# Optimization experiments

Measured on AMD Instinct MI355X. Metric: run time of the kernel, lower is better.

## Reference

```python
import jax, jax.numpy as jnp
import numpy as np
from jax import lax

BN_EPS = 1e-5

def _conv1d_same(x, w):
    # x: [N, 1, C], w: [1, 1, k] with k odd -> SAME padding along channel axis
    k = w.shape[-1]
    return lax.conv_general_dilated(x, w, window_strides=(1,),
                                    padding=[(k // 2, k // 2)],
                                    dimension_numbers=('NCH', 'OIH', 'NCH'))

def setup_inputs() -> dict:
    key = jax.random.key(0)
    ks = jax.random.split(key, 6)
    B, C, H, W = 4, 64, 64, 64
    kk = 3  # kernel size from in_dim=64: t=int(abs(log2(64)+1)/2)=3 (odd)
    x = jax.random.normal(ks[0], (B, C, H, W), dtype=jnp.float32)
    q_w = jax.random.normal(ks[1], (1, 1, kk), dtype=jnp.float32) * 0.5
    k_w = jax.random.normal(ks[2], (1, 1, kk), dtype=jnp.float32) * 0.5
    v_w = jax.random.normal(ks[3], (C, C), dtype=jnp.float32) * (1.0 / np.sqrt(C))
    v_b = jnp.zeros((C,), dtype=jnp.float32)
    gamma = jax.random.uniform(ks[4], (1,), dtype=jnp.float32, minval=0.5, maxval=1.5)
    bn_w = jnp.ones((C,), dtype=jnp.float32)
    bn_b = jnp.zeros((C,), dtype=jnp.float32)
    return {"x": x, "q_w": q_w, "k_w": k_w, "v_w": v_w, "v_b": v_b,
            "gamma": gamma, "bn_w": bn_w, "bn_b": bn_b}

def reference(x, q_w, k_w, v_w, v_b, gamma, bn_w, bn_b):
    B, C, H, W = x.shape
    N = H * W
    # conv1d Q/K projections over the channel axis, per spatial position
    xp = x.reshape(B, C, N).transpose(0, 2, 1).reshape(B * N, 1, C)
    q = _conv1d_same(xp, q_w).reshape(B, N, C)   # proj_query: [B, HW, C]
    k = _conv1d_same(xp, k_w).reshape(B, N, C)   # proj_key (pre-permute)
    energy = jnp.einsum('bnc,bmc->bnm', q, k)    # [B, HW, HW]
    attn = jax.nn.softmax(energy, axis=-1)
    # 1x1 value conv
    v = jnp.einsum('oc,bchw->bohw', v_w, x) + v_b[None, :, None, None]
    vv = v.reshape(B, C, N)
    # bmm(value, attention^T)
    out = jnp.einsum('bcm,bnm->bcn', vv, attn).reshape(B, C, H, W)
    y = gamma[0] * out
    # BatchNorm2d, training mode (batch statistics, biased variance)
    mean = jnp.mean(y, axis=(0, 2, 3), keepdims=True)
    var = jnp.var(y, axis=(0, 2, 3), keepdims=True)
    y = (y - mean) * lax.rsqrt(var + BN_EPS)
    y = y * bn_w[None, :, None, None] + bn_b[None, :, None, None]
    return y + x
```

## Files before the change

kernel.cpp:

```cpp
#include <hip/hip_runtime.h>
#include <stdint.h>

using f16 = _Float16;

typedef _Float16 f16x8 __attribute__((ext_vector_type(8)));
typedef float f32x4 __attribute__((ext_vector_type(4)));

#define LOG2E 1.44269504088896340736f

__device__ __forceinline__ f16 f2h(float f) { return (f16)f; }

#if __has_builtin(__builtin_amdgcn_exp2f)
__device__ __forceinline__ float fexp2(float x) { return __builtin_amdgcn_exp2f(x); }
#else
__device__ __forceinline__ float fexp2(float x) { return exp2f(x); }
#endif

typedef __attribute__((address_space(1))) const uint32_t gu32;
typedef __attribute__((address_space(3))) uint32_t lu32;

__device__ __forceinline__ void dma16(const void* g, void* l) {
  __builtin_amdgcn_global_load_lds((gu32*)g, (lu32*)l, 16, 0, 0);
}

__device__ __forceinline__ f16x8 cvt8(const float* p) {
  const float4 a = *(const float4*)p;
  const float4 b = *(const float4*)(p + 4);
  f16x8 r;
  r[0] = (f16)a.x; r[1] = (f16)a.y; r[2] = (f16)a.z; r[3] = (f16)a.w;
  r[4] = (f16)b.x; r[5] = (f16)b.y; r[6] = (f16)b.z; r[7] = (f16)b.w;
  return r;
}


__global__ __launch_bounds__(256, 2) void pam_pre(
    const float* __restrict__ x, const float* __restrict__ qw,
    const float* __restrict__ kw, const float* __restrict__ vw,
    const float* __restrict__ vb,
    f16* __restrict__ qa, f16* __restrict__ ka2, f16* __restrict__ va2,
    float* __restrict__ gz)
{
  __shared__ alignas(16) f16 xt[32 * 72];
  const int tid = threadIdx.x;
  const int b = blockIdx.x >> 7;
  const int n0 = (blockIdx.x & 127) << 5;
  const int lane = tid & 63;
  const int wv = tid >> 6;
  const int quad = lane >> 4, l15 = lane & 15;

  if (blockIdx.x == 0 && tid < 128) gz[tid] = 0.f;

  {
    const int c = tid >> 2;
    const int j0 = (tid & 3) << 3;
    const float* xp = x + ((size_t)(b * 64 + c) << 12) + n0 + j0;
    const float4 v0 = *(const float4*)xp;
    const float4 v1 = *(const float4*)(xp + 4);
    xt[(j0 + 0) * 72 + c] = f2h(v0.x);
    xt[(j0 + 1) * 72 + c] = f2h(v0.y);
    xt[(j0 + 2) * 72 + c] = f2h(v0.z);
    xt[(j0 + 3) * 72 + c] = f2h(v0.w);
    xt[(j0 + 4) * 72 + c] = f2h(v1.x);
    xt[(j0 + 5) * 72 + c] = f2h(v1.y);
    xt[(j0 + 6) * 72 + c] = f2h(v1.z);
    xt[(j0 + 7) * 72 + c] = f2h(v1.w);
  }
  __syncthreads();

  const float qw0 = qw[0], qw1 = qw[1], qw2 = qw[2];
  const float kw0 = kw[0], kw1 = kw[1], kw2 = kw[2];
  for (int p = 0; p < 8; ++p) {
    const int c = lane;
    const int jr = (p << 2) + wv;
    const int n = n0 + jr;
    const float xm = (c > 0) ? (float)xt[jr * 72 + c - 1] : 0.f;
    const float x0 = (float)xt[jr * 72 + c];
    const float xp = (c < 63) ? (float)xt[jr * 72 + c + 1] : 0.f;
    const float qv = (qw0 * xm + qw1 * x0 + qw2 * xp) * LOG2E;
    const float kv = kw0 * xm + kw1 * x0 + kw2 * xp;
    qa[((size_t)((b << 12) + n) << 6) + c] = f2h(qv);
    ka2[((size_t)(b * 8 + (c >> 3)) << 15) + (n << 3) + (c & 7)] = f2h(kv);
  }

  {
    const f16x8 a0 = cvt8(vw + (wv * 16 + l15) * 64 + quad * 8);
    const f16x8 a1 = cvt8(vw + (wv * 16 + l15) * 64 + quad * 8 + 32);
    f32x4 acc[2];
    for (int st = 0; st < 2; ++st) {
      const f16x8 b0 = *(const f16x8*)&xt[(st * 16 + l15) * 72 + quad * 8];
      const f16x8 b1 = *(const f16x8*)&xt[(st * 16 + l15) * 72 + quad * 8 + 32];
      f32x4 z = {0.f, 0.f, 0.f, 0.f};
      z = __builtin_amdgcn_mfma_f32_16x16x32_f16(a0, b0, z, 0, 0, 0);
      acc[st] = __builtin_amdgcn_mfma_f32_16x16x32_f16(a1, b1, z, 0, 0, 0);
    }
    const int cobase = wv * 16 + quad * 4;
    for (int st = 0; st < 2; ++st)
      for (int r = 0; r < 4; ++r) {
        const int co = cobase + r;
        const int n = n0 + st * 16 + l15;
        const float val = acc[st][r] + vb[co];
        va2[((size_t)(b * 512 + (n >> 3)) << 9) + (co << 3) + (n & 7)] = f2h(val);
      }
  }
}

__global__ __launch_bounds__(1024) void pam_attn(
    const f16* __restrict__ qa, const f16* __restrict__ ka2,
    const f16* __restrict__ va2, const float* __restrict__ gam,
    float* __restrict__ y0, float* __restrict__ gs1, float* __restrict__ gs2)
{
  __shared__ alignas(16) f16 kbuf[2][8192];
  __shared__ alignas(16) f16 vbuf[2][8192];
  __shared__ alignas(16) f16 pbuf[16][512];
  __shared__ float ldsO[64 * 65];
  __shared__ float ldsM[4][64], ldsL[4][64], ldsMg[64], ldsInv[64];

  const int tid = threadIdx.x;
  const int wv = tid >> 6, lane = tid & 63;
  const int quad = lane >> 4, l15 = lane & 15;
  const int qt = wv & 3, ks = wv >> 2;
  const int b = blockIdx.x & 3;
  const int qb = blockIdx.x >> 2;
  const int qb0 = qb << 6;
  const int phase = qb & 31;

  for (int i = tid; i < 64 * 65; i += 1024) ldsO[i] = 0.f;

  const int bn = b << 12;
  f16x8 bq0, bq1;
  {
    const int q = qb0 + qt * 16 + l15;
    const f16* qp = qa + ((size_t)(bn + q) << 6) + quad * 8;
    bq0 = *(const f16x8*)qp;
    bq1 = *(const f16x8*)(qp + 32);
  }

  const int k_c8 = tid >> 7, k_key = tid & 127;
  const f16* kg0 = ka2 + (((size_t)(b * 8 + k_c8)) << 15) + (k_key << 3);
  const int v_kc = tid >> 6, v_c = tid & 63;
  const f16* vg0 = va2 + (((size_t)(b * 512 + v_kc)) << 9) + (v_c << 3);

  const int ak_base = (((quad << 7) + ks * 32 + l15) << 3);
  const int bv_base = (((((ks << 2) + quad) << 6) + l15) << 3);

  f32x4 o[4] = {};
  float m = -1e30f, lp = 0.f;
  f16* pb = pbuf[wv];
  const int sw = l15 & 3;

  dma16(kg0 + ((size_t)phase << 10), kbuf[0] + (wv << 9));
  dma16(vg0 + ((size_t)phase << 13), vbuf[0] + (wv << 9));
  __syncthreads();

#pragma unroll 1
  for (int kt = 0; kt < 32; ++kt) {
    const int cur = kt & 1;
    {
      const int tn = (kt + 1 + phase) & 31;
      dma16(kg0 + ((size_t)tn << 10), kbuf[cur ^ 1] + (wv << 9));
      dma16(vg0 + ((size_t)tn << 13), vbuf[cur ^ 1] + (wv << 9));
    }

    const f16* kc_ = kbuf[cur];
    const f16* vc_ = vbuf[cur];
    const f16x8 ak00 = *(const f16x8*)(kc_ + ak_base);
    const f16x8 ak01 = *(const f16x8*)(kc_ + ak_base + 4096);
    const f16x8 ak10 = *(const f16x8*)(kc_ + ak_base + 128);
    const f16x8 ak11 = *(const f16x8*)(kc_ + ak_base + 128 + 4096);
    f16x8 bv[4];
    for (int ct = 0; ct < 4; ++ct)
      bv[ct] = *(const f16x8*)(vc_ + bv_base + ct * 128);

    f32x4 s0, s1;
    {
      f32x4 z = {0.f, 0.f, 0.f, 0.f};
      z = __builtin_amdgcn_mfma_f32_16x16x32_f16(ak00, bq0, z, 0, 0, 0);
      s0 = __builtin_amdgcn_mfma_f32_16x16x32_f16(ak01, bq1, z, 0, 0, 0);
    }
    {
      f32x4 z = {0.f, 0.f, 0.f, 0.f};
      z = __builtin_amdgcn_mfma_f32_16x16x32_f16(ak10, bq0, z, 0, 0, 0);
      s1 = __builtin_amdgcn_mfma_f32_16x16x32_f16(ak11, bq1, z, 0, 0, 0);
    }

    float tmax = fmaxf(fmaxf(fmaxf(s0[0], s0[1]), fmaxf(s0[2], s0[3])),
                       fmaxf(fmaxf(s1[0], s1[1]), fmaxf(s1[2], s1[3])));
    tmax = fmaxf(tmax, __shfl_xor(tmax, 16, 64));
    tmax = fmaxf(tmax, __shfl_xor(tmax, 32, 64));
    const bool upd = tmax > m;
    const float mnew = upd ? tmax : m;

    char* rowp = (char*)pb + l15 * 64;
    float tsum = 0.f;
    {
      const float p0 = fexp2(s0[0] - mnew);
      const float p1 = fexp2(s0[1] - mnew);
      const float p2 = fexp2(s0[2] - mnew);
      const float p3 = fexp2(s0[3] - mnew);
      tsum += (p0 + p1) + (p2 + p3);
      union { f16 h[4]; uint2 u; } pk;
      pk.h[0] = f2h(p0); pk.h[1] = f2h(p1);
      pk.h[2] = f2h(p2); pk.h[3] = f2h(p3);
      const int cc = (quad >> 1) ^ sw;
      *(uint2*)(rowp + cc * 16 + (quad & 1) * 8) = pk.u;
    }
    {
      const float p0 = fexp2(s1[0] - mnew);
      const float p1 = fexp2(s1[1] - mnew);
      const float p2 = fexp2(s1[2] - mnew);
      const float p3 = fexp2(s1[3] - mnew);
      tsum += (p0 + p1) + (p2 + p3);
      union { f16 h[4]; uint2 u; } pk;
      pk.h[0] = f2h(p0); pk.h[1] = f2h(p1);
      pk.h[2] = f2h(p2); pk.h[3] = f2h(p3);
      const int cc = (2 + (quad >> 1)) ^ sw;
      *(uint2*)(rowp + cc * 16 + (quad & 1) * 8) = pk.u;
    }

    if (__any(upd)) {
      const float alpha = fexp2(m - mnew);
      lp = lp * alpha + tsum;
      const int srcbase = (lane & 48) + ((lane >> 4) << 2);
      for (int r = 0; r < 4; ++r) {
        const float ar = __shfl(alpha, srcbase + r, 64);
        for (int ct = 0; ct < 4; ++ct) o[ct][r] *= ar;
      }
    } else {
      lp += tsum;
    }
    m = mnew;
    __builtin_amdgcn_s_waitcnt(0xC07F);

    const f16x8 ap =
        *(const f16x8*)((const char*)pb + l15 * 64 + ((quad ^ sw) << 4));
    for (int ct = 0; ct < 4; ++ct)
      o[ct] = __builtin_amdgcn_mfma_f32_16x16x32_f16(ap, bv[ct], o[ct], 0, 0, 0);

    __syncthreads();
  }

  {
    float v = lp;
    v += __shfl_xor(v, 16, 64);
    v += __shfl_xor(v, 32, 64);
    if (quad == 0) {
      ldsM[ks][qt * 16 + l15] = m;
      ldsL[ks][qt * 16 + l15] = v;
    }
  }
  __syncthreads();

  if (tid < 64) {
    const float M = fmaxf(fmaxf(ldsM[0][tid], ldsM[1][tid]),
                          fmaxf(ldsM[2][tid], ldsM[3][tid]));
    const float lt = ldsL[0][tid] * fexp2(ldsM[0][tid] - M) +
                     ldsL[1][tid] * fexp2(ldsM[1][tid] - M) +
                     ldsL[2][tid] * fexp2(ldsM[2][tid] - M) +
                     ldsL[3][tid] * fexp2(ldsM[3][tid] - M);
    ldsMg[tid] = M;
    ldsInv[tid] = 1.f / lt;
  }
  __syncthreads();

  for (int r = 0; r < 4; ++r) {
    const int q = qt * 16 + quad * 4 + r;
    const float sc = fexp2(ldsM[ks][q] - ldsMg[q]);
    for (int ct = 0; ct < 4; ++ct)
      atomicAdd(&ldsO[q * 65 + ct * 16 + l15], o[ct][r] * sc);
  }
  __syncthreads();

  const float g = gam[0];
  {
    const int c = tid >> 4;
    const int q0 = (tid & 15) << 2;
    float4 v4;
    float* vp = &v4.x;
    float s1 = 0.f, s2 = 0.f;
    for (int r = 0; r < 4; ++r) {
      const float val = g * ldsO[(q0 + r) * 65 + c] * ldsInv[q0 + r];
      vp[r] = val; s1 += val; s2 += val * val;
    }
    *(float4*)(y0 + ((size_t)(b * 64 + c) << 12) + qb0 + q0) = v4;
    s1 += __shfl_xor(s1, 1, 64);
    s2 += __shfl_xor(s2, 1, 64);
    s1 += __shfl_xor(s1, 2, 64);
    s2 += __shfl_xor(s2, 2, 64);
    s1 += __shfl_xor(s1, 4, 64);
    s2 += __shfl_xor(s2, 4, 64);
    s1 += __shfl_xor(s1, 8, 64);
    s2 += __shfl_xor(s2, 8, 64);
    if (l15 == 0) {
      atomicAdd(&gs1[c], s1);
      atomicAdd(&gs2[c], s2);
    }
  }
}

__global__ __launch_bounds__(256, 2) void pam_apply(
    const float* __restrict__ y0, const float* __restrict__ x,
    const float* __restrict__ gs1, const float* __restrict__ gs2,
    const float* __restrict__ bnw, const float* __restrict__ bnb,
    float* __restrict__ out)
{
  const int i = (blockIdx.x * 256 + threadIdx.x) << 2;
  const int c = (i >> 12) & 63;
  const float inv_n = 1.f / 16384.f;
  const float mean = gs1[c] * inv_n;
  const float var = fmaxf(gs2[c] * inv_n - mean * mean, 0.f);
  const float sc = bnw[c] * rsqrtf(var + 1e-5f);
  const float sh = bnb[c] - mean * sc;
  const float4 y = *(const float4*)(y0 + i);
  const float4 xv = *(const float4*)(x + i);
  float4 r;
  r.x = y.x * sc + sh + xv.x;
  r.y = y.y * sc + sh + xv.y;
  r.z = y.z * sc + sh + xv.z;
  r.w = y.w * sc + sh + xv.w;
  *(float4*)(out + i) = r;
}

extern "C" void kernel_launch(void* const* d_in, const int* in_sizes, int n_in,
                              void* d_out, int out_size, void* d_ws, size_t ws_size,
                              hipStream_t stream)
{
  (void)in_sizes; (void)n_in; (void)out_size; (void)ws_size;
  const float* x   = (const float*)d_in[0];
  const float* qw  = (const float*)d_in[1];
  const float* kw  = (const float*)d_in[2];
  const float* vw  = (const float*)d_in[3];
  const float* vb  = (const float*)d_in[4];
  const float* gam = (const float*)d_in[5];
  const float* bnw = (const float*)d_in[6];
  const float* bnb = (const float*)d_in[7];

  char* ws = (char*)d_ws;
  f16*   qa  = (f16*)(ws);
  f16*   ka2 = (f16*)(ws + (2u << 20));
  f16*   va2 = (f16*)(ws + (4u << 20));
  float* y0  = (float*)(ws + (6u << 20));
  float* gs1 = (float*)(ws + (10u << 20));
  float* gs2 = (float*)(ws + (10u << 20) + 256);

  pam_pre  <<<512, 256, 0, stream>>>(x, qw, kw, vw, vb, qa, ka2, va2, gs1);
  pam_attn <<<256, 1024, 0, stream>>>(qa, ka2, va2, gam, y0, gs1, gs2);
  pam_apply<<<1024, 256, 0, stream>>>(y0, x, gs1, gs2, bnw, bnb, (float*)d_out);
}
```

Before: 162.5 us.

## Keep softmax probabilities in registers and double key tile per iteration

The attention kernel now processes 256-key tiles over 16 iterations. Each wave handles two query tiles against 32 keys, so each K/V fragment loaded from LDS is reused twice. Probabilities are fed directly from the MFMA accumulator layout into 16x16x16 MFMAs as the A operand, which removes the per-wave P round-trip through LDS. The V layout is changed to groups of 4 keys to match that operand shape. Risks include doubled LDS staging buffers (about 128KB), more registers for two accumulator sets, and an 8-way cross-wave merge instead of 4.

```diff
diff --git a/kernel.cpp b/kernel.cpp
--- a/kernel.cpp
+++ b/kernel.cpp
@@ -4,6 +4,7 @@
 using f16 = _Float16;
 
 typedef _Float16 f16x8 __attribute__((ext_vector_type(8)));
+typedef _Float16 f16x4 __attribute__((ext_vector_type(4)));
 typedef float f32x4 __attribute__((ext_vector_type(4)));
 
 #define LOG2E 1.44269504088896340736f
@@ -37,7 +38,7 @@
     const float* __restrict__ x, const float* __restrict__ qw,
     const float* __restrict__ kw, const float* __restrict__ vw,
     const float* __restrict__ vb,
-    f16* __restrict__ qa, f16* __restrict__ ka2, f16* __restrict__ va2,
+    f16* __restrict__ qa, f16* __restrict__ ka2, f16* __restrict__ va3,
     float* __restrict__ gz)
 {
   __shared__ alignas(16) f16 xt[32 * 72];
@@ -99,174 +100,175 @@
         const int co = cobase + r;
         const int n = n0 + st * 16 + l15;
         const float val = acc[st][r] + vb[co];
-        va2[((size_t)(b * 512 + (n >> 3)) << 9) + (co << 3) + (n & 7)] = f2h(val);
-      }
-  }
-}
-
-__global__ __launch_bounds__(1024) void pam_attn(
+        va3[(((size_t)(b * 1024 + (n >> 2))) << 8) + (co << 2) + (n & 3)] = f2h(val);
+      }
+  }
+}
+
+__global__ __launch_bounds__(1024, 4) void pam_attn(
     const f16* __restrict__ qa, const f16* __restrict__ ka2,
-    const f16* __restrict__ va2, const float* __restrict__ gam,
+    const f16* __restrict__ va3, const float* __restrict__ gam,
     float* __restrict__ y0, float* __restrict__ gs1, float* __restrict__ gs2)
 {
-  __shared__ alignas(16) f16 kbuf[2][8192];
-  __shared__ alignas(16) f16 vbuf[2][8192];
-  __shared__ alignas(16) f16 pbuf[16][512];
+  __shared__ alignas(16) f16 kbuf[2][16384];
+  __shared__ alignas(16) f16 vbuf[2][16384];
   __shared__ float ldsO[64 * 65];
-  __shared__ float ldsM[4][64], ldsL[4][64], ldsMg[64], ldsInv[64];
+  __shared__ float ldsM[8][64], ldsL[8][64], ldsMg[64], ldsInv[64];
 
   const int tid = threadIdx.x;
   const int wv = tid >> 6, lane = tid & 63;
   const int quad = lane >> 4, l15 = lane & 15;
-  const int qt = wv & 3, ks = wv >> 2;
+  const int ks = wv & 7, qh = wv >> 3;
   const int b = blockIdx.x & 3;
   const int qb = blockIdx.x >> 2;
   const int qb0 = qb << 6;
-  const int phase = qb & 31;
+  const int phase = qb & 15;
 
   for (int i = tid; i < 64 * 65; i += 1024) ldsO[i] = 0.f;
 
   const int bn = b << 12;
-  f16x8 bq0, bq1;
-  {
-    const int q = qb0 + qt * 16 + l15;
+  f16x8 bq[2][2];
+  for (int qt = 0; qt < 2; ++qt) {
+    const int q = qb0 + (qh * 2 + qt) * 16 + l15;
     const f16* qp = qa + ((size_t)(bn + q) << 6) + quad * 8;
-    bq0 = *(const f16x8*)qp;
-    bq1 = *(const f16x8*)(qp + 32);
-  }
-
-  const int k_c8 = tid >> 7, k_key = tid & 127;
-  const f16* kg0 = ka2 + (((size_t)(b * 8 + k_c8)) << 15) + (k_key << 3);
-  const int v_kc = tid >> 6, v_c = tid & 63;
-  const f16* vg0 = va2 + (((size_t)(b * 512 + v_kc)) << 9) + (v_c << 3);
-
-  const int ak_base = (((quad << 7) + ks * 32 + l15) << 3);
-  const int bv_base = (((((ks << 2) + quad) << 6) + l15) << 3);
-
-  f32x4 o[4] = {};
-  float m = -1e30f, lp = 0.f;
-  f16* pb = pbuf[wv];
-  const int sw = l15 & 3;
-
-  dma16(kg0 + ((size_t)phase << 10), kbuf[0] + (wv << 9));
-  dma16(vg0 + ((size_t)phase << 13), vbuf[0] + (wv << 9));
+    bq[qt][0] = *(const f16x8*)qp;
+    bq[qt][1] = *(const f16x8*)(qp + 32);
+  }
+
+  const int k_c8 = wv >> 1;
+  const int k_koff = (wv & 1) << 7;
+  const f16* kg0 = ka2 + (((size_t)(b * 8 + k_c8)) << 15) + (k_koff << 3) + (lane << 3);
+  const int kl_base = k_c8 * 2048 + (k_koff << 3);
+  const f16* vg0 = va3 + ((size_t)b << 18) + ((wv * 64 + lane) << 3);
+  const int vl_base = wv << 9;
+
+  f32x4 o[2][4] = {};
+  float m[2] = {-1e30f, -1e30f};
+  float lp[2] = {0.f, 0.f};
+
+  dma16(kg0 + ((size_t)phase << 11),        kbuf[0] + kl_base);
+  dma16(kg0 + ((size_t)phase << 11) + 512,  kbuf[0] + kl_base + 512);
+  dma16(vg0 + ((size_t)phase << 14),        vbuf[0] + vl_base);
+  dma16(vg0 + ((size_t)phase << 14) + 8192, vbuf[0] + vl_base + 8192);
   __syncthreads();
 
 #pragma unroll 1
-  for (int kt = 0; kt < 32; ++kt) {
+  for (int kt = 0; kt < 16; ++kt) {
     const int cur = kt & 1;
     {
-      const int tn = (kt + 1 + phase) & 31;
-      dma16(kg0 + ((size_t)tn << 10), kbuf[cur ^ 1] + (wv << 9));
-      dma16(vg0 + ((size_t)tn << 13), vbuf[cur ^ 1] + (wv << 9));
-    }
-
-    const f16* kc_ = kbuf[cur];
-    const f16* vc_ = vbuf[cur];
-    const f16x8 ak00 = *(const f16x8*)(kc_ + ak_base);
-    const f16x8 ak01 = *(const f16x8*)(kc_ + ak_base + 4096);
-    const f16x8 ak10 = *(const f16x8*)(kc_ + ak_base + 128);
-    const f16x8 ak11 = *(const f16x8*)(kc_ + ak_base + 128 + 4096);
-    f16x8 bv[4];
-    for (int ct = 0; ct < 4; ++ct)
-      bv[ct] = *(const f16x8*)(vc_ + bv_base + ct * 128);
-
-    f32x4 s0, s1;
-    {
-      f32x4 z = {0.f, 0.f, 0.f, 0.f};
-      z = __builtin_amdgcn_mfma_f32_16x16x32_f16(ak00, bq0, z, 0, 0, 0);
-      s0 = __builtin_amdgcn_mfma_f32_16x16x32_f16(ak01, bq1, z, 0, 0, 0);
-    }
-    {
-      f32x4 z = {0.f, 0.f, 0.f, 0.f};
-      z = __builtin_amdgcn_mfma_f32_16x16x32_f16(ak10, bq0, z, 0, 0, 0);
-      s1 = __builtin_amdgcn_mfma_f32_16x16x32_f16(ak11, bq1, z, 0, 0, 0);
-    }
-
-    float tmax = fmaxf(fmaxf(fmaxf(s0[0], s0[1]), fmaxf(s0[2], s0[3])),
-                       fmaxf(fmaxf(s1[0], s1[1]), fmaxf(s1[2], s1[3])));
-    tmax = fmaxf(tmax, __shfl_xor(tmax, 16, 64));
-    tmax = fmaxf(tmax, __shfl_xor(tmax, 32, 64));
-    const bool upd = tmax > m;
-    const float mnew = upd ? tmax : m;
-
-    char* rowp = (char*)pb + l15 * 64;
-    float tsum = 0.f;
-    {
-      const float p0 = fexp2(s0[0] - mnew);
-      const float p1 = fexp2(s0[1] - mnew);
-      const float p2 = fexp2(s0[2] - mnew);
-      const float p3 = fexp2(s0[3] - mnew);
-      tsum += (p0 + p1) + (p2 + p3);
-      union { f16 h[4]; uint2 u; } pk;
-      pk.h[0] = f2h(p0); pk.h[1] = f2h(p1);
-      pk.h[2] = f2h(p2); pk.h[3] = f2h(p3);
-      const int cc = (quad >> 1) ^ sw;
-      *(uint2*)(rowp + cc * 16 + (quad & 1) * 8) = pk.u;
-    }
-    {
-      const float p0 = fexp2(s1[0] - mnew);
-      const float p1 = fexp2(s1[1] - mnew);
-      const float p2 = fexp2(s1[2] - mnew);
-      const float p3 = fexp2(s1[3] - mnew);
-      tsum += (p0 + p1) + (p2 + p3);
-      union { f16 h[4]; uint2 u; } pk;
-      pk.h[0] = f2h(p0); pk.h[1] = f2h(p1);
-      pk.h[2] = f2h(p2); pk.h[3] = f2h(p3);
-      const int cc = (2 + (quad >> 1)) ^ sw;
-      *(uint2*)(rowp + cc * 16 + (quad & 1) * 8) = pk.u;
-    }
-
-    if (__any(upd)) {
-      const float alpha = fexp2(m - mnew);
-      lp = lp * alpha + tsum;
-      const int srcbase = (lane & 48) + ((lane >> 4) << 2);
-      for (int r = 0; r < 4; ++r) {
-        const float ar = __shfl(alpha, srcbase + r, 64);
-        for (int ct = 0; ct < 4; ++ct) o[ct][r] *= ar;
-      }
-    } else {
-      lp += tsum;
-    }
-    m = mnew;
-    __builtin_amdgcn_s_waitcnt(0xC07F);
-
-    const f16x8 ap =
-        *(const f16x8*)((const char*)pb + l15 * 64 + ((quad ^ sw) << 4));
-    for (int ct = 0; ct < 4; ++ct)
-      o[ct] = __builtin_amdgcn_mfma_f32_16x16x32_f16(ap, bv[ct], o[ct], 0, 0, 0);
-
+      const int tn = (kt + 1 + phase) & 15;
+      f16* kd = kbuf[cur ^ 1] + kl_base;
+      f16* vd = vbuf[cur ^ 1] + vl_base;
+      dma16(kg0 + ((size_t)tn << 11),        kd);
+      dma16(kg0 + ((size_t)tn << 11) + 512,  kd + 512);
+      dma16(vg0 + ((size_t)tn << 14),        vd);
+      dma16(vg0 + ((size_t)tn << 14) + 8192, vd + 8192);
+    }
+
+    const f16* kc = kbuf[cur];
+    const f16* vc = vbuf[cur];
+    f16x8 ak[2][2];
+    for (int mt = 0; mt < 2; ++mt) {
+      const int keyL = (ks * 32 + mt * 16 + l15) << 3;
+      ak[mt][0] = *(const f16x8*)(kc + quad * 2048 + keyL);
+      ak[mt][1] = *(const f16x8*)(kc + (4 + quad) * 2048 + keyL);
+    }
+
+    f16x4 a[2][2];
+    for (int qt = 0; qt < 2; ++qt) {
+      f32x4 s0, s1;
+      {
+        f32x4 z = {0.f, 0.f, 0.f, 0.f};
+        z = __builtin_amdgcn_mfma_f32_16x16x32_f16(ak[0][0], bq[qt][0], z, 0, 0, 0);
+        s0 = __builtin_amdgcn_mfma_f32_16x16x32_f16(ak[0][1], bq[qt][1], z, 0, 0, 0);
+      }
+      {
+        f32x4 z = {0.f, 0.f, 0.f, 0.f};
+        z = __builtin_amdgcn_mfma_f32_16x16x32_f16(ak[1][0], bq[qt][0], z, 0, 0, 0);
+        s1 = __builtin_amdgcn_mfma_f32_16x16x32_f16(ak[1][1], bq[qt][1], z, 0, 0, 0);
+      }
+
+      float tmax = fmaxf(fmaxf(fmaxf(s0[0], s0[1]), fmaxf(s0[2], s0[3])),
+                         fmaxf(fmaxf(s1[0], s1[1]), fmaxf(s1[2], s1[3])));
+      tmax = fmaxf(tmax, __shfl_xor(tmax, 16, 64));
+      tmax = fmaxf(tmax, __shfl_xor(tmax, 32, 64));
+      const bool upd = tmax > m[qt];
+      const float mnew = upd ? tmax : m[qt];
+
+      float tsum = 0.f;
+      {
+        const float p0 = fexp2(s0[0] - mnew);
+        const float p1 = fexp2(s0[1] - mnew);
+        const float p2 = fexp2(s0[2] - mnew);
+        const float p3 = fexp2(s0[3] - mnew);
+        tsum += (p0 + p1) + (p2 + p3);
+        a[qt][0][0] = f2h(p0); a[qt][0][1] = f2h(p1);
+        a[qt][0][2] = f2h(p2); a[qt][0][3] = f2h(p3);
+      }
+      {
+        const float p0 = fexp2(s1[0] - mnew);
+        const float p1 = fexp2(s1[1] - mnew);
+        const float p2 = fexp2(s1[2] - mnew);
+        const float p3 = fexp2(s1[3] - mnew);
+        tsum += (p0 + p1) + (p2 + p3);
+        a[qt][1][0] = f2h(p0); a[qt][1][1] = f2h(p1);
+        a[qt][1][2] = f2h(p2); a[qt][1][3] = f2h(p3);
+      }
+
+      if (__any(upd)) {
+        const float alpha = fexp2(m[qt] - mnew);
+        lp[qt] = lp[qt] * alpha + tsum;
+        const int srcbase = (lane & 48) + ((lane >> 4) << 2);
+        for (int r = 0; r < 4; ++r) {
+          const float ar = __shfl(alpha, srcbase + r, 64);
+          for (int ct = 0; ct < 4; ++ct) o[qt][ct][r] *= ar;
+        }
+      } else {
+        lp[qt] += tsum;
+      }
+      m[qt] = mnew;
+    }
+
+    for (int ct = 0; ct < 4; ++ct) {
+      const int cb = ((ct * 16 + l15) << 2);
+      const f16x4 bv0 = *(const f16x4*)(vc + ((ks * 8 + quad) << 8) + cb);
+      const f16x4 bv1 = *(const f16x4*)(vc + ((ks * 8 + 4 + quad) << 8) + cb);
+      for (int qt = 0; qt < 2; ++qt) {
+        o[qt][ct] = __builtin_amdgcn_mfma_f32_16x16x16f16(a[qt][0], bv0, o[qt][ct], 0, 0, 0);
+        o[qt][ct] = __builtin_amdgcn_mfma_f32_16x16x16f16(a[qt][1], bv1, o[qt][ct], 0, 0, 0);
+      }
+    }
     __syncthreads();
   }
 
-  {
-    float v = lp;
+  for (int qt = 0; qt < 2; ++qt) {
+    float v = lp[qt];
     v += __shfl_xor(v, 16, 64);
     v += __shfl_xor(v, 32, 64);
     if (quad == 0) {
-      ldsM[ks][qt * 16 + l15] = m;
-      ldsL[ks][qt * 16 + l15] = v;
+      ldsM[ks][(qh * 2 + qt) * 16 + l15] = m[qt];
+      ldsL[ks][(qh * 2 + qt) * 16 + l15] = v;
     }
   }
   __syncthreads();
 
   if (tid < 64) {
-    const float M = fmaxf(fmaxf(ldsM[0][tid], ldsM[1][tid]),
-                          fmaxf(ldsM[2][tid], ldsM[3][tid]));
-    const float lt = ldsL[0][tid] * fexp2(ldsM[0][tid] - M) +
-                     ldsL[1][tid] * fexp2(ldsM[1][tid] - M) +
-                     ldsL[2][tid] * fexp2(ldsM[2][tid] - M) +
-                     ldsL[3][tid] * fexp2(ldsM[3][tid] - M);
+    float M = ldsM[0][tid];
+    for (int w = 1; w < 8; ++w) M = fmaxf(M, ldsM[w][tid]);
+    float lt = 0.f;
+    for (int w = 0; w < 8; ++w) lt += ldsL[w][tid] * fexp2(ldsM[w][tid] - M);
     ldsMg[tid] = M;
     ldsInv[tid] = 1.f / lt;
   }
   __syncthreads();
 
-  for (int r = 0; r < 4; ++r) {
-    const int q = qt * 16 + quad * 4 + r;
-    const float sc = fexp2(ldsM[ks][q] - ldsMg[q]);
-    for (int ct = 0; ct < 4; ++ct)
-      atomicAdd(&ldsO[q * 65 + ct * 16 + l15], o[ct][r] * sc);
+  for (int qt = 0; qt < 2; ++qt) {
+    for (int r = 0; r < 4; ++r) {
+      const int q = (qh * 2 + qt) * 16 + quad * 4 + r;
+      const float sc = fexp2(ldsM[ks][q] - ldsMg[q]);
+      for (int ct = 0; ct < 4; ++ct)
+        atomicAdd(&ldsO[q * 65 + ct * 16 + l15], o[qt][ct][r] * sc);
+    }
   }
   __syncthreads();
 
@@ -337,12 +339,12 @@
   char* ws = (char*)d_ws;
   f16*   qa  = (f16*)(ws);
   f16*   ka2 = (f16*)(ws + (2u << 20));
-  f16*   va2 = (f16*)(ws + (4u << 20));
+  f16*   va3 = (f16*)(ws + (4u << 20));
   float* y0  = (float*)(ws + (6u << 20));
   float* gs1 = (float*)(ws + (10u << 20));
   float* gs2 = (float*)(ws + (10u << 20) + 256);
 
-  pam_pre  <<<512, 256, 0, stream>>>(x, qw, kw, vw, vb, qa, ka2, va2, gs1);
-  pam_attn <<<256, 1024, 0, stream>>>(qa, ka2, va2, gam, y0, gs1, gs2);
+  pam_pre  <<<512, 256, 0, stream>>>(x, qw, kw, vw, vb, qa, ka2, va3, gs1);
+  pam_attn <<<256, 1024, 0, stream>>>(qa, ka2, va3, gam, y0, gs1, gs2);
   pam_apply<<<1024, 256, 0, stream>>>(y0, x, gs1, gs2, bnw, bnb, (float*)d_out);
 }
```

Result: slower. 180.9 us (+11.3%).

## Keep softmax probabilities in registers and halve attention block query tile

Applied to the files above, without the earlier changes.

The attention kernel no longer round-trips the probability tile through LDS. The S accumulator layout is fed directly as the A operand of 16x16x16 MFMAs, which requires a new V layout grouped by 4 keys (va3) produced by the pre kernel. Blocks now handle 32 queries with 512 threads and two blocks per CU, doubling the grid and raising occupancy. The cost is each block re-streaming the full K/V for half as many queries, which doubles global/L2 traffic for K and V, and using the smaller MFMA shape.

```diff
diff --git a/kernel.cpp b/kernel.cpp
--- a/kernel.cpp
+++ b/kernel.cpp
@@ -4,6 +4,7 @@
 using f16 = _Float16;
 
 typedef _Float16 f16x8 __attribute__((ext_vector_type(8)));
+typedef _Float16 f16x4 __attribute__((ext_vector_type(4)));
 typedef float f32x4 __attribute__((ext_vector_type(4)));
 
 #define LOG2E 1.44269504088896340736f
@@ -37,13 +38,13 @@
     const float* __restrict__ x, const float* __restrict__ qw,
     const float* __restrict__ kw, const float* __restrict__ vw,
     const float* __restrict__ vb,
-    f16* __restrict__ qa, f16* __restrict__ ka2, f16* __restrict__ va2,
+    f16* __restrict__ qa, f16* __restrict__ ka2, f16* __restrict__ va3,
     float* __restrict__ gz)
 {
-  __shared__ alignas(16) f16 xt[32 * 72];
+  __shared__ alignas(16) f16 xt[16 * 72];
   const int tid = threadIdx.x;
-  const int b = blockIdx.x >> 7;
-  const int n0 = (blockIdx.x & 127) << 5;
+  const int b = blockIdx.x >> 8;
+  const int n0 = (blockIdx.x & 255) << 4;
   const int lane = tid & 63;
   const int wv = tid >> 6;
   const int quad = lane >> 4, l15 = lane & 15;
@@ -52,24 +53,18 @@
 
   {
     const int c = tid >> 2;
-    const int j0 = (tid & 3) << 3;
-    const float* xp = x + ((size_t)(b * 64 + c) << 12) + n0 + j0;
-    const float4 v0 = *(const float4*)xp;
-    const float4 v1 = *(const float4*)(xp + 4);
+    const int j0 = (tid & 3) << 2;
+    const float4 v0 = *(const float4*)(x + ((size_t)(b * 64 + c) << 12) + n0 + j0);
     xt[(j0 + 0) * 72 + c] = f2h(v0.x);
     xt[(j0 + 1) * 72 + c] = f2h(v0.y);
     xt[(j0 + 2) * 72 + c] = f2h(v0.z);
     xt[(j0 + 3) * 72 + c] = f2h(v0.w);
-    xt[(j0 + 4) * 72 + c] = f2h(v1.x);
-    xt[(j0 + 5) * 72 + c] = f2h(v1.y);
-    xt[(j0 + 6) * 72 + c] = f2h(v1.z);
-    xt[(j0 + 7) * 72 + c] = f2h(v1.w);
   }
   __syncthreads();
 
   const float qw0 = qw[0], qw1 = qw[1], qw2 = qw[2];
   const float kw0 = kw[0], kw1 = kw[1], kw2 = kw[2];
-  for (int p = 0; p < 8; ++p) {
+  for (int p = 0; p < 4; ++p) {
     const int c = lane;
     const int jr = (p << 2) + wv;
     const int n = n0 + jr;
@@ -85,71 +80,61 @@
   {
     const f16x8 a0 = cvt8(vw + (wv * 16 + l15) * 64 + quad * 8);
     const f16x8 a1 = cvt8(vw + (wv * 16 + l15) * 64 + quad * 8 + 32);
-    f32x4 acc[2];
-    for (int st = 0; st < 2; ++st) {
-      const f16x8 b0 = *(const f16x8*)&xt[(st * 16 + l15) * 72 + quad * 8];
-      const f16x8 b1 = *(const f16x8*)&xt[(st * 16 + l15) * 72 + quad * 8 + 32];
-      f32x4 z = {0.f, 0.f, 0.f, 0.f};
-      z = __builtin_amdgcn_mfma_f32_16x16x32_f16(a0, b0, z, 0, 0, 0);
-      acc[st] = __builtin_amdgcn_mfma_f32_16x16x32_f16(a1, b1, z, 0, 0, 0);
-    }
+    const f16x8 b0 = *(const f16x8*)&xt[l15 * 72 + quad * 8];
+    const f16x8 b1 = *(const f16x8*)&xt[l15 * 72 + quad * 8 + 32];
+    f32x4 z = {0.f, 0.f, 0.f, 0.f};
+    z = __builtin_amdgcn_mfma_f32_16x16x32_f16(a0, b0, z, 0, 0, 0);
+    z = __builtin_amdgcn_mfma_f32_16x16x32_f16(a1, b1, z, 0, 0, 0);
     const int cobase = wv * 16 + quad * 4;
-    for (int st = 0; st < 2; ++st)
-      for (int r = 0; r < 4; ++r) {
-        const int co = cobase + r;
-        const int n = n0 + st * 16 + l15;
-        const float val = acc[st][r] + vb[co];
-        va2[((size_t)(b * 512 + (n >> 3)) << 9) + (co << 3) + (n & 7)] = f2h(val);
-      }
-  }
-}
-
-__global__ __launch_bounds__(1024) void pam_attn(
+    for (int r = 0; r < 4; ++r) {
+      const int co = cobase + r;
+      const int n = n0 + l15;
+      const float val = z[r] + vb[co];
+      va3[(((size_t)(b * 1024 + (n >> 2))) << 8) + (co << 2) + (n & 3)] = f2h(val);
+    }
+  }
+}
+
+__global__ __launch_bounds__(512, 2) void pam_attn(
     const f16* __restrict__ qa, const f16* __restrict__ ka2,
-    const f16* __restrict__ va2, const float* __restrict__ gam,
+    const f16* __restrict__ va3, const float* __restrict__ gam,
     float* __restrict__ y0, float* __restrict__ gs1, float* __restrict__ gs2)
 {
   __shared__ alignas(16) f16 kbuf[2][8192];
   __shared__ alignas(16) f16 vbuf[2][8192];
-  __shared__ alignas(16) f16 pbuf[16][512];
-  __shared__ float ldsO[64 * 65];
-  __shared__ float ldsM[4][64], ldsL[4][64], ldsMg[64], ldsInv[64];
+  __shared__ float ldsO[32 * 65];
+  __shared__ float ldsM[4][32], ldsL[4][32], ldsMg[32], ldsInv[32];
 
   const int tid = threadIdx.x;
   const int wv = tid >> 6, lane = tid & 63;
   const int quad = lane >> 4, l15 = lane & 15;
-  const int qt = wv & 3, ks = wv >> 2;
+  const int ks = wv & 3, qh = wv >> 2;
   const int b = blockIdx.x & 3;
   const int qb = blockIdx.x >> 2;
-  const int qb0 = qb << 6;
+  const int qb0 = qb << 5;
   const int phase = qb & 31;
 
-  for (int i = tid; i < 64 * 65; i += 1024) ldsO[i] = 0.f;
+  for (int i = tid; i < 32 * 65; i += 512) ldsO[i] = 0.f;
 
   const int bn = b << 12;
   f16x8 bq0, bq1;
   {
-    const int q = qb0 + qt * 16 + l15;
+    const int q = qb0 + qh * 16 + l15;
     const f16* qp = qa + ((size_t)(bn + q) << 6) + quad * 8;
     bq0 = *(const f16x8*)qp;
     bq1 = *(const f16x8*)(qp + 32);
   }
 
-  const int k_c8 = tid >> 7, k_key = tid & 127;
-  const f16* kg0 = ka2 + (((size_t)(b * 8 + k_c8)) << 15) + (k_key << 3);
-  const int v_kc = tid >> 6, v_c = tid & 63;
-  const f16* vg0 = va2 + (((size_t)(b * 512 + v_kc)) << 9) + (v_c << 3);
-
-  const int ak_base = (((quad << 7) + ks * 32 + l15) << 3);
-  const int bv_base = (((((ks << 2) + quad) << 6) + l15) << 3);
+  const f16* kg0 = ka2 + (((size_t)(b * 8 + wv)) << 15) + (lane << 3);
+  const f16* vg0 = va3 + ((size_t)b << 18) + (wv << 10) + (lane << 3);
 
   f32x4 o[4] = {};
   float m = -1e30f, lp = 0.f;
-  f16* pb = pbuf[wv];
-  const int sw = l15 & 3;
-
-  dma16(kg0 + ((size_t)phase << 10), kbuf[0] + (wv << 9));
-  dma16(vg0 + ((size_t)phase << 13), vbuf[0] + (wv << 9));
+
+  dma16(kg0 + ((size_t)phase << 10),       kbuf[0] + (wv << 10));
+  dma16(kg0 + ((size_t)phase << 10) + 512, kbuf[0] + (wv << 10) + 512);
+  dma16(vg0 + ((size_t)phase << 13),       vbuf[0] + (wv << 10));
+  dma16(vg0 + ((size_t)phase << 13) + 512, vbuf[0] + (wv << 10) + 512);
   __syncthreads();
 
 #pragma unroll 1
@@ -157,19 +142,22 @@
     const int cur = kt & 1;
     {
       const int tn = (kt + 1 + phase) & 31;
-      dma16(kg0 + ((size_t)tn << 10), kbuf[cur ^ 1] + (wv << 9));
-      dma16(vg0 + ((size_t)tn << 13), vbuf[cur ^ 1] + (wv << 9));
-    }
-
-    const f16* kc_ = kbuf[cur];
-    const f16* vc_ = vbuf[cur];
-    const f16x8 ak00 = *(const f16x8*)(kc_ + ak_base);
-    const f16x8 ak01 = *(const f16x8*)(kc_ + ak_base + 4096);
-    const f16x8 ak10 = *(const f16x8*)(kc_ + ak_base + 128);
-    const f16x8 ak11 = *(const f16x8*)(kc_ + ak_base + 128 + 4096);
-    f16x8 bv[4];
-    for (int ct = 0; ct < 4; ++ct)
-      bv[ct] = *(const f16x8*)(vc_ + bv_base + ct * 128);
+      f16* kd = kbuf[cur ^ 1] + (wv << 10);
+      f16* vd = vbuf[cur ^ 1] + (wv << 10);
+      dma16(kg0 + ((size_t)tn << 10),       kd);
+      dma16(kg0 + ((size_t)tn << 10) + 512, kd + 512);
+      dma16(vg0 + ((size_t)tn << 13),       vd);
+      dma16(vg0 + ((size_t)tn << 13) + 512, vd + 512);
+    }
+
+    const f16* kc = kbuf[cur];
+    const f16* vc = vbuf[cur];
+    const int keyL0 = (ks * 32 + l15) << 3;
+    const int keyL1 = (ks * 32 + 16 + l15) << 3;
+    const f16x8 ak00 = *(const f16x8*)(kc + quad * 1024 + keyL0);
+    const f16x8 ak01 = *(const f16x8*)(kc + (4 + quad) * 1024 + keyL0);
+    const f16x8 ak10 = *(const f16x8*)(kc + quad * 1024 + keyL1);
+    const f16x8 ak11 = *(const f16x8*)(kc + (4 + quad) * 1024 + keyL1);
 
     f32x4 s0, s1;
     {
@@ -190,7 +178,7 @@
     const bool upd = tmax > m;
     const float mnew = upd ? tmax : m;
 
-    char* rowp = (char*)pb + l15 * 64;
+    f16x4 a0, a1;
     float tsum = 0.f;
     {
       const float p0 = fexp2(s0[0] - mnew);
@@ -198,11 +186,7 @@
       const float p2 = fexp2(s0[2] - mnew);
       const float p3 = fexp2(s0[3] - mnew);
       tsum += (p0 + p1) + (p2 + p3);
-      union { f16 h[4]; uint2 u; } pk;
-      pk.h[0] = f2h(p0); pk.h[1] = f2h(p1);
-      pk.h[2] = f2h(p2); pk.h[3] = f2h(p3);
-      const int cc = (quad >> 1) ^ sw;
-      *(uint2*)(rowp + cc * 16 + (quad & 1) * 8) = pk.u;
+      a0[0] = f2h(p0); a0[1] = f2h(p1); a0[2] = f2h(p2); a0[3] = f2h(p3);
     }
     {
       const float p0 = fexp2(s1[0] - mnew);
@@ -210,11 +194,7 @@
       const float p2 = fexp2(s1[2] - mnew);
       const float p3 = fexp2(s1[3] - mnew);
       tsum += (p0 + p1) + (p2 + p3);
-      union { f16 h[4]; uint2 u; } pk;
-      pk.h[0] = f2h(p0); pk.h[1] = f2h(p1);
-      pk.h[2] = f2h(p2); pk.h[3] = f2h(p3);
-      const int cc = (2 + (quad >> 1)) ^ sw;
-      *(uint2*)(rowp + cc * 16 + (quad & 1) * 8) = pk.u;
+      a1[0] = f2h(p0); a1[1] = f2h(p1); a1[2] = f2h(p2); a1[3] = f2h(p3);
     }
 
     if (__any(upd)) {
@@ -229,13 +209,14 @@
       lp += tsum;
     }
     m = mnew;
-    __builtin_amdgcn_s_waitcnt(0xC07F);
-
-    const f16x8 ap =
-        *(const f16x8*)((const char*)pb + l15 * 64 + ((quad ^ sw) << 4));
-    for (int ct = 0; ct < 4; ++ct)
-      o[ct] = __builtin_amdgcn_mfma_f32_16x16x32_f16(ap, bv[ct], o[ct], 0, 0, 0);
-
+
+    for (int ct = 0; ct < 4; ++ct) {
+      const int cb = (ct * 16 + l15) << 2;
+      const f16x4 bv0 = *(const f16x4*)(vc + ((ks * 8 + quad) << 8) + cb);
+      const f16x4 bv1 = *(const f16x4*)(vc + ((ks * 8 + 4 + quad) << 8) + cb);
+      o[ct] = __builtin_amdgcn_mfma_f32_16x16x16f16(a0, bv0, o[ct], 0, 0, 0);
+      o[ct] = __builtin_amdgcn_mfma_f32_16x16x16f16(a1, bv1, o[ct], 0, 0, 0);
+    }
     __syncthreads();
   }
 
@@ -244,13 +225,13 @@
     v += __shfl_xor(v, 16, 64);
     v += __shfl_xor(v, 32, 64);
     if (quad == 0) {
-      ldsM[ks][qt * 16 + l15] = m;
-      ldsL[ks][qt * 16 + l15] = v;
-    }
-  }
-  __syncthreads();
-
-  if (tid < 64) {
+      ldsM[ks][qh * 16 + l15] = m;
+      ldsL[ks][qh * 16 + l15] = v;
+    }
+  }
+  __syncthreads();
+
+  if (tid < 32) {
     const float M = fmaxf(fmaxf(ldsM[0][tid], ldsM[1][tid]),
                           fmaxf(ldsM[2][tid], ldsM[3][tid]));
     const float lt = ldsL[0][tid] * fexp2(ldsM[0][tid] - M) +
@@ -263,7 +244,7 @@
   __syncthreads();
 
   for (int r = 0; r < 4; ++r) {
-    const int q = qt * 16 + quad * 4 + r;
+    const int q = qh * 16 + quad * 4 + r;
     const float sc = fexp2(ldsM[ks][q] - ldsMg[q]);
     for (int ct = 0; ct < 4; ++ct)
       atomicAdd(&ldsO[q * 65 + ct * 16 + l15], o[ct][r] * sc);
@@ -272,8 +253,8 @@
 
   const float g = gam[0];
   {
-    const int c = tid >> 4;
-    const int q0 = (tid & 15) << 2;
+    const int c = tid >> 3;
+    const int q0 = (tid & 7) << 2;
     float4 v4;
     float* vp = &v4.x;
     float s1 = 0.f, s2 = 0.f;
@@ -288,9 +269,7 @@
     s2 += __shfl_xor(s2, 2, 64);
     s1 += __shfl_xor(s1, 4, 64);
     s2 += __shfl_xor(s2, 4, 64);
-    s1 += __shfl_xor(s1, 8, 64);
-    s2 += __shfl_xor(s2, 8, 64);
-    if (l15 == 0) {
+    if ((tid & 7) == 0) {
       atomicAdd(&gs1[c], s1);
       atomicAdd(&gs2[c], s2);
     }
@@ -337,12 +316,12 @@
   char* ws = (char*)d_ws;
   f16*   qa  = (f16*)(ws);
   f16*   ka2 = (f16*)(ws + (2u << 20));
-  f16*   va2 = (f16*)(ws + (4u << 20));
+  f16*   va3 = (f16*)(ws + (4u << 20));
   float* y0  = (float*)(ws + (6u << 20));
   float* gs1 = (float*)(ws + (10u << 20));
   float* gs2 = (float*)(ws + (10u << 20) + 256);
 
-  pam_pre  <<<512, 256, 0, stream>>>(x, qw, kw, vw, vb, qa, ka2, va2, gs1);
-  pam_attn <<<256, 1024, 0, stream>>>(qa, ka2, va2, gam, y0, gs1, gs2);
+  pam_pre  <<<1024, 256, 0, stream>>>(x, qw, kw, vw, vb, qa, ka2, va3, gs1);
+  pam_attn <<<512, 512, 0, stream>>>(qa, ka2, va3, gam, y0, gs1, gs2);
   pam_apply<<<1024, 256, 0, stream>>>(y0, x, gs1, gs2, bnw, bnb, (float*)d_out);
 }
```

Measured after the change: 152.9 us. 1.06x faster.
